# Kernel tuning notes

Hardware: AMD Instinct MI355X
Metric: run time of the kernel (lower is better)

## Reference

```python
import jax, jax.numpy as jnp
import numpy as np

DELTA = 0.0  # default `delta` arg of forward


def _features(voxels, clust_ids, num_clusters):
    # voxels: [N,3] float, clust_ids: [N] int in [0, C)
    n = voxels.shape[0]
    seg = lambda x: jax.ops.segment_sum(x, clust_ids, num_segments=num_clusters)
    counts = seg(jnp.ones((n,), voxels.dtype))                     # [C] cluster sizes
    safe_cnt = jnp.maximum(counts, 1.0)
    center = seg(voxels) / safe_cnt[:, None]                       # [C,3] per-cluster mean
    xc = voxels - center[clust_ids]                                # [N,3] centered voxels
    cov = seg(xc[:, :, None] * xc[:, None, :])                     # [C,3,3] = x^T x per cluster
    w, v = jnp.linalg.eigh(cov)                                    # eigvals ascending (== torch.eig + argsort)
    w2 = w[:, 2]
    dirwt = jnp.where(w2 == 0, 0.0, 1.0 - w[:, 1] / jnp.where(w2 == 0, 1.0, w2))
    wd = w + DELTA
    denom = jnp.where(wd[:, 2] == 0, 1.0, wd[:, 2])
    wn = wd / denom[:, None]                                       # w normalized by largest
    eye = jnp.eye(3, dtype=voxels.dtype)
    B = (1.0 - DELTA) * jnp.einsum('cij,cj,ckj->cik', v, wn, v) + DELTA * eye  # [C,3,3]
    v0 = v[:, :, 2]                                                # [C,3] principal axis
    x0 = jnp.sum(xc * v0[clust_ids], axis=-1)                      # [N] projection on v0
    xp0 = xc - x0[:, None] * v0[clust_ids]                         # [N,3] residual
    np0 = jnp.linalg.norm(xp0, axis=1)                             # [N]
    sc = seg(x0 * np0)                                             # [C] sign score
    v0 = jnp.where((sc < 0)[:, None], -v0, v0) * dirwt[:, None]
    # len(c) < 2 branch: center = the voxel itself (mean handles it), B = delta*I, v0 = 0
    small = counts < 2.0
    B = jnp.where(small[:, None, None], DELTA * eye, B)
    v0 = jnp.where(small[:, None], 0.0, v0)
    return jnp.concatenate([center, B.reshape(num_clusters, 9), v0, counts[:, None]], axis=1)  # [C,16]


def setup_inputs() -> dict:
    key = jax.random.key(0)
    k1, k2 = jax.random.split(key)
    n, c = 4000000, 4096
    data = jax.random.normal(k1, (n, 5), dtype=jnp.float32)
    clust_ids = jax.random.randint(k2, (n,), 0, c)
    return {"data": data, "clust_ids": clust_ids, "num_clusters": c}


def reference(data, clust_ids, num_clusters):
    voxels = data[:, :3].astype(jnp.float32)
    return _features(voxels, clust_ids, num_clusters)
```

## Files before the change

### kernel.cpp

```cpp
#include <hip/hip_runtime.h>
#include <math.h>

#define NC 4096
#define OVCAP 131072
#define CAP1 8520

__device__ __forceinline__ int xcd_id() {
    return (int)__builtin_amdgcn_s_getreg(20 | (0 << 6) | ((4 - 1) << 11));
}

__device__ __forceinline__ void solve_cluster(const float mom[10], float* o,
                                              float4* pcv, float4* pvv) {
    float cntf = mom[0];
    double dn  = (double)cntf;
    double inv = 1.0 / fmax(dn, 1.0);
    double cx = mom[1] * inv, cy = mom[2] * inv, cz = mom[3] * inv;

    double a00 = (double)mom[4] - dn * cx * cx;
    double a01 = (double)mom[5] - dn * cx * cy;
    double a02 = (double)mom[6] - dn * cx * cz;
    double a11 = (double)mom[7] - dn * cy * cy;
    double a12 = (double)mom[8] - dn * cy * cz;
    double a22 = (double)mom[9] - dn * cz * cz;

    double q  = (a00 + a11 + a22) / 3.0;
    double p1 = a01 * a01 + a02 * a02 + a12 * a12;
    double b00 = a00 - q, b11 = a11 - q, b22 = a22 - q;
    double p2 = b00 * b00 + b11 * b11 + b22 * b22 + 2.0 * p1;
    double w0, w1, w2;
    if (!(p2 > 0.0)) {
        w0 = w1 = w2 = q;
    } else {
        double p  = sqrt(p2 / 6.0);
        double ip = 1.0 / p;
        double c00 = b00 * ip, c01 = a01 * ip, c02 = a02 * ip;
        double c11 = b11 * ip, c12 = a12 * ip, c22 = b22 * ip;
        double detB = c00 * (c11 * c22 - c12 * c12)
                    - c01 * (c01 * c22 - c12 * c02)
                    + c02 * (c01 * c12 - c11 * c02);
        double r = fmin(1.0, fmax(-1.0, detB * 0.5));
        double phi = acos(r) / 3.0;
        w2 = q + 2.0 * p * cos(phi);
        w0 = q + 2.0 * p * cos(phi + 2.0943951023931953);
        w1 = 3.0 * q - w2 - w0;
    }

    double denom = (w2 == 0.0) ? 1.0 : w2;
    double dirwt = (w2 == 0.0) ? 0.0 : (1.0 - w1 / w2);

    double C00 = a00 - w1, C11 = a11 - w1, C22 = a22 - w1;
    double D00 = a00 - w0, D11 = a11 - w0, D22 = a22 - w0;
    double M00 = C00 * D00 + a01 * a01 + a02 * a02;
    double M10 = a01 * D00 + C11 * a01 + a12 * a02;
    double M20 = a02 * D00 + a12 * a01 + C22 * a02;
    double M01 = C00 * a01 + a01 * D11 + a02 * a12;
    double M11 = a01 * a01 + C11 * D11 + a12 * a12;
    double M21 = a02 * a01 + a12 * D11 + C22 * a12;
    double M02 = C00 * a02 + a01 * a12 + a02 * D22;
    double M12 = a01 * a02 + C11 * a12 + a12 * D22;
    double M22 = a02 * a02 + a12 * a12 + C22 * D22;
    double n0 = M00 * M00 + M10 * M10 + M20 * M20;
    double n1 = M01 * M01 + M11 * M11 + M21 * M21;
    double n2 = M02 * M02 + M12 * M12 + M22 * M22;
    double vx, vy, vz, nn;
    if (n0 >= n1 && n0 >= n2) { vx = M00; vy = M10; vz = M20; nn = n0; }
    else if (n1 >= n2)        { vx = M01; vy = M11; vz = M21; nn = n1; }
    else                      { vx = M02; vy = M12; vz = M22; nn = n2; }
    if (nn > 1e-300) {
        double rn = 1.0 / sqrt(nn);
        vx *= rn; vy *= rn; vz *= rn;
    } else {
        vx = vy = vz = 0.0;
    }

    bool small = cntf < 2.0f;
    float bscale = small ? 0.0f : (float)(1.0 / denom);

    o[0]  = (float)cx;
    o[1]  = (float)cy;
    o[2]  = (float)cz;
    o[3]  = (float)a00 * bscale;
    o[4]  = (float)a01 * bscale;
    o[5]  = (float)a02 * bscale;
    o[6]  = (float)a01 * bscale;
    o[7]  = (float)a11 * bscale;
    o[8]  = (float)a12 * bscale;
    o[9]  = (float)a02 * bscale;
    o[10] = (float)a12 * bscale;
    o[11] = (float)a22 * bscale;
    o[15] = cntf;

    *pcv = make_float4((float)cx, (float)cy, (float)cz, (float)dirwt);
    *pvv = make_float4((float)vx, (float)vy, (float)vz, cntf);
}

__device__ __forceinline__ void ov_spill(float4 d, int id, float4* ov, int* novf,
                                         float* gmom) {
    int ovi = atomicAdd(novf, 1);
    if (ovi < OVCAP) ov[ovi] = d;
    atomicAdd(&gmom[0 * NC + id], 1.0f);
    atomicAdd(&gmom[1 * NC + id], d.x);
    atomicAdd(&gmom[2 * NC + id], d.y);
    atomicAdd(&gmom[3 * NC + id], d.z);
    atomicAdd(&gmom[4 * NC + id], d.x * d.x);
    atomicAdd(&gmom[5 * NC + id], d.x * d.y);
    atomicAdd(&gmom[6 * NC + id], d.x * d.z);
    atomicAdd(&gmom[7 * NC + id], d.y * d.y);
    atomicAdd(&gmom[8 * NC + id], d.y * d.z);
    atomicAdd(&gmom[9 * NC + id], d.z * d.z);
}

__global__ __launch_bounds__(512) void k_p1(const float* __restrict__ data,
                                            const int* __restrict__ ids,
                                            float4* __restrict__ P1,
                                            int* __restrict__ cnt1,
                                            float4* __restrict__ ov,
                                            int* __restrict__ novf,
                                            float* __restrict__ gmom, int n) {
    __shared__ float sbuf[6144];
    __shared__ unsigned short sid[2048];
    __shared__ int h64[64], boff[64], bglob[64];
    float* sx = sbuf;
    float* sy = sbuf + 2048;
    float* sz = sbuf + 4096;
    int tid = threadIdx.x, lane = tid & 63;
    int xcd = xcd_id() & 7;
    int ntiles = (n + 2047) >> 11;
    for (int t = blockIdx.x; t < ntiles; t += gridDim.x) {
        int vbase = t << 11;
        if (tid < 64) h64[tid] = 0;
        __syncthreads();
        float vx[4], vy[4], vz[4];
        int vid[4], vrk[4];
#pragma unroll
        for (int s = 0; s < 4; s++) {
            int v = vbase + (s << 9) + tid;
            if (v < n) {
                vx[s] = data[v * 5 + 0];
                vy[s] = data[v * 5 + 1];
                vz[s] = data[v * 5 + 2];
                int id = ids[v];
                vid[s] = id;
                vrk[s] = atomicAdd(&h64[id >> 6], 1);
            } else vid[s] = -1;
        }
        __syncthreads();
        if (tid < 64) {
            int c0 = h64[tid], sc = c0;
            for (int off = 1; off < 64; off <<= 1) {
                int u = __shfl_up(sc, off);
                if (lane >= off) sc += u;
            }
            boff[tid] = sc - c0;
            bglob[tid] = atomicAdd(&cnt1[((tid << 3) + xcd) << 4], c0);
        }
        __syncthreads();
#pragma unroll
        for (int s = 0; s < 4; s++)
            if (vid[s] >= 0) {
                int p = boff[vid[s] >> 6] + vrk[s];
                sx[p] = vx[s]; sy[p] = vy[s]; sz[p] = vz[s];
                sid[p] = (unsigned short)vid[s];
            }
        __syncthreads();
        int tot = n - vbase;
        tot = tot > 2048 ? 2048 : tot;
        for (int i = tid; i < tot; i += 512) {
            int id = (int)sid[i];
            int b = id >> 6;
            int ofs = bglob[b] + (i - boff[b]);
            float4 d = make_float4(sx[i], sy[i], sz[i], __int_as_float(id));
            if (ofs < CAP1)
                P1[(size_t)((b << 3) + xcd) * CAP1 + ofs] = d;
            else
                ov_spill(d, id, ov, novf, gmom);
        }
        __syncthreads();
    }
}

__global__ __launch_bounds__(512) void k_mom(const float4* __restrict__ P1,
                                             const int* __restrict__ cnt1,
                                             float* __restrict__ gmom) {
    __shared__ float sbuf[6144];
    __shared__ int h64[64], boff[64];
    float* sx = sbuf;
    float* sy = sbuf + 2048;
    float* sz = sbuf + 4096;
    int tid = threadIdx.x, lane = tid & 63, w8 = tid >> 6;
    int xcd = blockIdx.x & 7;
    int rest = blockIdx.x >> 3;
    int bucket = rest & 63;
    int q = rest >> 6;
    int sub = (bucket << 3) + xcd;

    int m1c = cnt1[sub << 4];
    m1c = m1c > CAP1 ? CAP1 : m1c;
    int start = (int)(((long long)m1c * q) >> 1);
    int end   = (int)(((long long)m1c * (q + 1)) >> 1);
    size_t sbase = (size_t)sub * CAP1;

    float creg = 0.0f;
    float m1 = 0, m2 = 0, m3 = 0, m4 = 0, m5 = 0, m6 = 0, m7 = 0, m8 = 0, m9 = 0;

    for (int tb = start; tb < end; tb += 2048) {
        if (tid < 64) h64[tid] = 0;
        __syncthreads();
        float4 vd[4];
        int vcid[4], vrk[4];
#pragma unroll
        for (int s = 0; s < 4; s++) {
            int i = tb + (s << 9) + tid;
            if (i < end) {
                float4 d = P1[sbase + i];
                int cid = __float_as_int(d.w) & 63;
                vd[s] = d; vcid[s] = cid;
                vrk[s] = atomicAdd(&h64[cid], 1);
            } else vcid[s] = -1;
        }
        __syncthreads();
        if (tid < 64) {
            int c0 = h64[tid], sc = c0;
            for (int off = 1; off < 64; off <<= 1) {
                int u = __shfl_up(sc, off);
                if (lane >= off) sc += u;
            }
            boff[tid] = sc - c0;
        }
        __syncthreads();
#pragma unroll
        for (int s = 0; s < 4; s++)
            if (vcid[s] >= 0) {
                int p = boff[vcid[s]] + vrk[s];
                sx[p] = vd[s].x; sy[p] = vd[s].y; sz[p] = vd[s].z;
            }
        __syncthreads();
        int len = h64[lane];
        int bo  = boff[lane];
        if (w8 == 0) creg += (float)len;
        for (int j = w8; j < len; j += 8) {
            float x = sx[bo + j], y = sy[bo + j], z = sz[bo + j];
            m1 += x; m2 += y; m3 += z;
            m4 += x * x; m5 += x * y; m6 += x * z;
            m7 += y * y; m8 += y * z; m9 += z * z;
        }
        __syncthreads();
    }

    float* comb = sbuf;
    float regs[10] = {creg, m1, m2, m3, m4, m5, m6, m7, m8, m9};
#pragma unroll
    for (int k = 0; k < 10; k++)
        comb[(((k << 6) + lane) << 3) + w8] = regs[k];
    __syncthreads();
    for (int i = tid; i < 640; i += 512) {
        int k = i >> 6, c = i & 63;
        float* p = comb + (((k << 6) + c) << 3);
        float v = ((p[0] + p[1]) + (p[2] + p[3])) + ((p[4] + p[5]) + (p[6] + p[7]));
        if (v != 0.0f) atomicAdd(&gmom[k * NC + (bucket << 6) + c], v);
    }
}

__global__ __launch_bounds__(256) void k_scp(const float4* __restrict__ P1,
                                             const int* __restrict__ cnt1,
                                             const float4* __restrict__ pcv,
                                             const float4* __restrict__ ov,
                                             const int* __restrict__ novf,
                                             float* __restrict__ gsc) {
    __shared__ float ssc[2][64];
    int tid = threadIdx.x;
    int half = tid >> 7;
    int xcd = blockIdx.x & 7;
    int rest = blockIdx.x >> 3;
    int bucket = rest & 63;
    int q = rest >> 6;
    int sub = (bucket << 3) + xcd;
    if (tid < 128) ssc[tid >> 6][tid & 63] = 0.0f;
    __syncthreads();
    int m1 = cnt1[sub << 4];
    m1 = m1 > CAP1 ? CAP1 : m1;
    int start = (int)(((long long)m1 * q) >> 2);
    int end   = (int)(((long long)m1 * (q + 1)) >> 2);
    size_t sbase = (size_t)sub * CAP1;
    const float4* tab = pcv + ((size_t)bucket << 7);

    for (int i = start + tid; i < end; i += 256) {
        float4 d = P1[sbase + i];
        int cid = __float_as_int(d.w) & 63;
        float4 c4 = tab[cid * 2];
        float4 v4 = tab[cid * 2 + 1];
        float xc = d.x - c4.x, yc = d.y - c4.y, zc = d.z - c4.z;
        float x0 = xc * v4.x + yc * v4.y + zc * v4.z;
        float px = xc - x0 * v4.x;
        float py = yc - x0 * v4.y;
        float pz = zc - x0 * v4.z;
        atomicAdd(&ssc[half][cid], x0 * sqrtf(px * px + py * py + pz * pz));
    }
    if (xcd == 0 && q == 0) {
        int mo = *novf;
        mo = mo > OVCAP ? OVCAP : mo;
        for (int i = tid; i < mo; i += 256) {
            float4 d = ov[i];
            int id = __float_as_int(d.w);
            if ((id >> 6) == bucket) {
                int cid = id & 63;
                float4 c4 = tab[cid * 2];
                float4 v4 = tab[cid * 2 + 1];
                float xc = d.x - c4.x, yc = d.y - c4.y, zc = d.z - c4.z;
                float x0 = xc * v4.x + yc * v4.y + zc * v4.z;
                float px = xc - x0 * v4.x;
                float py = yc - x0 * v4.y;
                float pz = zc - x0 * v4.z;
                atomicAdd(&ssc[half][cid], x0 * sqrtf(px * px + py * py + pz * pz));
            }
        }
    }
    __syncthreads();
    if (tid < 64) {
        float v = ssc[0][tid] + ssc[1][tid];
        if (v != 0.0f) atomicAdd(&gsc[(bucket << 6) + tid], v);
    }
}

__global__ void k_eigen_fb(const float* __restrict__ gmom, float* __restrict__ out,
                           float4* __restrict__ pcv) {
    int c = blockIdx.x * blockDim.x + threadIdx.x;
    if (c >= NC) return;
    float mom[10];
#pragma unroll
    for (int k = 0; k < 10; k++) mom[k] = gmom[k * NC + c];
    solve_cluster(mom, out + c * 16, &pcv[2 * c], &pcv[2 * c + 1]);
}

__global__ void k_final_fb(const float4* __restrict__ pcv,
                           const float* __restrict__ gsc, float* __restrict__ out) {
    int c = blockIdx.x * blockDim.x + threadIdx.x;
    if (c >= NC) return;
    float4 c4 = pcv[2 * c];
    float4 v4 = pcv[2 * c + 1];
    float s = (gsc[c] < 0.0f) ? -c4.w : c4.w;
    if (v4.w < 2.0f) s = 0.0f;
    out[c * 16 + 12] = v4.x * s;
    out[c * 16 + 13] = v4.y * s;
    out[c * 16 + 14] = v4.z * s;
}

__global__ __launch_bounds__(1024) void k_accum_raw(const float* __restrict__ data,
                                                    const int* __restrict__ ids,
                                                    float* __restrict__ gmom, int n) {
    extern __shared__ float s[];
    for (int i = threadIdx.x; i < 10 * NC; i += blockDim.x) s[i] = 0.0f;
    __syncthreads();
    int stride = gridDim.x * blockDim.x;
    for (int i = blockIdx.x * blockDim.x + threadIdx.x; i < n; i += stride) {
        int id = ids[i];
        float x = data[i * 5 + 0], y = data[i * 5 + 1], z = data[i * 5 + 2];
        atomicAdd(&s[0 * NC + id], 1.0f);
        atomicAdd(&s[1 * NC + id], x);
        atomicAdd(&s[2 * NC + id], y);
        atomicAdd(&s[3 * NC + id], z);
        atomicAdd(&s[4 * NC + id], x * x);
        atomicAdd(&s[5 * NC + id], x * y);
        atomicAdd(&s[6 * NC + id], x * z);
        atomicAdd(&s[7 * NC + id], y * y);
        atomicAdd(&s[8 * NC + id], y * z);
        atomicAdd(&s[9 * NC + id], z * z);
    }
    __syncthreads();
    for (int i = threadIdx.x; i < 10 * NC; i += blockDim.x) {
        float v = s[i];
        if (v != 0.0f) atomicAdd(&gmom[i], v);
    }
}

__global__ __launch_bounds__(1024) void k_sc_raw(const float* __restrict__ data,
                                                 const int* __restrict__ ids,
                                                 const float4* __restrict__ pcv,
                                                 float* __restrict__ gsc, int n) {
    extern __shared__ float4 sl4[];
    float4* spc = sl4;
    float4* spv = sl4 + NC;
    float*  ssc = (float*)(sl4 + 2 * NC);
    for (int i = threadIdx.x; i < NC; i += blockDim.x) {
        spc[i] = pcv[2 * i]; spv[i] = pcv[2 * i + 1]; ssc[i] = 0.0f;
    }
    __syncthreads();
    int stride = gridDim.x * blockDim.x;
    for (int i = blockIdx.x * blockDim.x + threadIdx.x; i < n; i += stride) {
        int id = ids[i];
        float4 c4 = spc[id];
        float4 v4 = spv[id];
        float xc = data[i * 5 + 0] - c4.x;
        float yc = data[i * 5 + 1] - c4.y;
        float zc = data[i * 5 + 2] - c4.z;
        float x0 = xc * v4.x + yc * v4.y + zc * v4.z;
        float px = xc - x0 * v4.x;
        float py = yc - x0 * v4.y;
        float pz = zc - x0 * v4.z;
        atomicAdd(&ssc[id], x0 * sqrtf(px * px + py * py + pz * pz));
    }
    __syncthreads();
    for (int i = threadIdx.x; i < NC; i += blockDim.x) {
        float v = ssc[i];
        if (v != 0.0f) atomicAdd(&gsc[i], v);
    }
}

extern "C" void kernel_launch(void* const* d_in, const int* in_sizes, int n_in,
                              void* d_out, int out_size, void* d_ws, size_t ws_size,
                              hipStream_t stream) {
    const float* data = (const float*)d_in[0];
    const int*   ids  = (const int*)d_in[1];
    float* out = (float*)d_out;
    int n = in_sizes[1];

    char* ws = (char*)d_ws;
    float*  gmom = (float*)(ws);
    float*  gsc  = (float*)(ws + 163840);
    int*    cnt1 = (int*)(ws + 180224);
    int*    novf = (int*)(ws + 212992);
    float4* pcv  = (float4*)(ws + 213056);
    float4* ov   = (float4*)(ws + 344128);
    const size_t FIXED = 2441280;
    const size_t P1SZ  = (size_t)512 * CAP1 * 16;

    if (ws_size >= FIXED + P1SZ) {
        float4* P1 = (float4*)(ws + FIXED);
        hipMemsetAsync(ws, 0, 213056, stream);
        hipLaunchKernelGGL(k_p1, dim3(1024), dim3(512), 0, stream,
                           data, ids, P1, cnt1, ov, novf, gmom, n);
        hipLaunchKernelGGL(k_mom, dim3(1024), dim3(512), 0, stream,
                           P1, cnt1, gmom);
        hipLaunchKernelGGL(k_eigen_fb, dim3(16), dim3(256), 0, stream,
                           gmom, out, pcv);
        hipLaunchKernelGGL(k_scp, dim3(2048), dim3(256), 0, stream,
                           P1, cnt1, pcv, ov, novf, gsc);
        hipLaunchKernelGGL(k_final_fb, dim3(16), dim3(256), 0, stream,
                           pcv, gsc, out);
    } else {
        hipMemsetAsync(ws, 0, 180224, stream);
        hipLaunchKernelGGL(k_accum_raw, dim3(256), dim3(1024), 10 * NC * 4, stream,
                           data, ids, gmom, n);
        hipLaunchKernelGGL(k_eigen_fb, dim3(16), dim3(256), 0, stream, gmom, out, pcv);
        hipLaunchKernelGGL(k_sc_raw, dim3(256), dim3(1024), 2 * NC * 16 + NC * 4, stream,
                           data, ids, pcv, gsc, n);
        hipLaunchKernelGGL(k_final_fb, dim3(16), dim3(256), 0, stream, pcv, gsc, out);
    }
}
```

Before: 188.6 us.

## Store bucketed points as SoA with 16-bit ids and double grid splits

The intermediate bucketed point buffer changes from float4 records (x,y,z,id) to separate x, y, z float arrays plus a 16-bit id array. This cuts the bytes written by the partition kernel and read by the moment and sign-score kernels from 16 to 14 per point. The moment and score kernels also split each sub-bucket into twice as many chunks with doubled grids, for more parallelism. The cost is four narrower scattered stores instead of one vector store, and more blocks doing atomic merges.

```diff
diff --git a/kernel.cpp b/kernel.cpp
--- a/kernel.cpp
+++ b/kernel.cpp
@@ -112,7 +112,10 @@
 
 __global__ __launch_bounds__(512) void k_p1(const float* __restrict__ data,
                                             const int* __restrict__ ids,
-                                            float4* __restrict__ P1,
+                                            float* __restrict__ P1x,
+                                            float* __restrict__ P1y,
+                                            float* __restrict__ P1z,
+                                            unsigned short* __restrict__ P1id,
                                             int* __restrict__ cnt1,
                                             float4* __restrict__ ov,
                                             int* __restrict__ novf,
@@ -169,17 +172,23 @@
             int id = (int)sid[i];
             int b = id >> 6;
             int ofs = bglob[b] + (i - boff[b]);
-            float4 d = make_float4(sx[i], sy[i], sz[i], __int_as_float(id));
-            if (ofs < CAP1)
-                P1[(size_t)((b << 3) + xcd) * CAP1 + ofs] = d;
-            else
-                ov_spill(d, id, ov, novf, gmom);
-        }
-        __syncthreads();
-    }
-}
-
-__global__ __launch_bounds__(512) void k_mom(const float4* __restrict__ P1,
+            if (ofs < CAP1) {
+                size_t o = (size_t)((b << 3) + xcd) * CAP1 + ofs;
+                P1x[o] = sx[i]; P1y[o] = sy[i]; P1z[o] = sz[i];
+                P1id[o] = (unsigned short)id;
+            } else {
+                ov_spill(make_float4(sx[i], sy[i], sz[i], __int_as_float(id)),
+                         id, ov, novf, gmom);
+            }
+        }
+        __syncthreads();
+    }
+}
+
+__global__ __launch_bounds__(512) void k_mom(const float* __restrict__ P1x,
+                                             const float* __restrict__ P1y,
+                                             const float* __restrict__ P1z,
+                                             const unsigned short* __restrict__ P1id,
                                              const int* __restrict__ cnt1,
                                              float* __restrict__ gmom) {
     __shared__ float sbuf[6144];
@@ -196,8 +205,8 @@
 
     int m1c = cnt1[sub << 4];
     m1c = m1c > CAP1 ? CAP1 : m1c;
-    int start = (int)(((long long)m1c * q) >> 1);
-    int end   = (int)(((long long)m1c * (q + 1)) >> 1);
+    int start = (int)(((long long)m1c * q) >> 2);
+    int end   = (int)(((long long)m1c * (q + 1)) >> 2);
     size_t sbase = (size_t)sub * CAP1;
 
     float creg = 0.0f;
@@ -206,15 +215,17 @@
     for (int tb = start; tb < end; tb += 2048) {
         if (tid < 64) h64[tid] = 0;
         __syncthreads();
-        float4 vd[4];
+        float vX[4], vY[4], vZ[4];
         int vcid[4], vrk[4];
 #pragma unroll
         for (int s = 0; s < 4; s++) {
             int i = tb + (s << 9) + tid;
             if (i < end) {
-                float4 d = P1[sbase + i];
-                int cid = __float_as_int(d.w) & 63;
-                vd[s] = d; vcid[s] = cid;
+                vX[s] = P1x[sbase + i];
+                vY[s] = P1y[sbase + i];
+                vZ[s] = P1z[sbase + i];
+                int cid = (int)P1id[sbase + i] & 63;
+                vcid[s] = cid;
                 vrk[s] = atomicAdd(&h64[cid], 1);
             } else vcid[s] = -1;
         }
@@ -232,7 +243,7 @@
         for (int s = 0; s < 4; s++)
             if (vcid[s] >= 0) {
                 int p = boff[vcid[s]] + vrk[s];
-                sx[p] = vd[s].x; sy[p] = vd[s].y; sz[p] = vd[s].z;
+                sx[p] = vX[s]; sy[p] = vY[s]; sz[p] = vZ[s];
             }
         __syncthreads();
         int len = h64[lane];
@@ -261,7 +272,10 @@
     }
 }
 
-__global__ __launch_bounds__(256) void k_scp(const float4* __restrict__ P1,
+__global__ __launch_bounds__(256) void k_scp(const float* __restrict__ P1x,
+                                             const float* __restrict__ P1y,
+                                             const float* __restrict__ P1z,
+                                             const unsigned short* __restrict__ P1id,
                                              const int* __restrict__ cnt1,
                                              const float4* __restrict__ pcv,
                                              const float4* __restrict__ ov,
@@ -279,17 +293,17 @@
     __syncthreads();
     int m1 = cnt1[sub << 4];
     m1 = m1 > CAP1 ? CAP1 : m1;
-    int start = (int)(((long long)m1 * q) >> 2);
-    int end   = (int)(((long long)m1 * (q + 1)) >> 2);
+    int start = (int)(((long long)m1 * q) >> 3);
+    int end   = (int)(((long long)m1 * (q + 1)) >> 3);
     size_t sbase = (size_t)sub * CAP1;
     const float4* tab = pcv + ((size_t)bucket << 7);
 
     for (int i = start + tid; i < end; i += 256) {
-        float4 d = P1[sbase + i];
-        int cid = __float_as_int(d.w) & 63;
+        float x = P1x[sbase + i], y = P1y[sbase + i], z = P1z[sbase + i];
+        int cid = (int)P1id[sbase + i] & 63;
         float4 c4 = tab[cid * 2];
         float4 v4 = tab[cid * 2 + 1];
-        float xc = d.x - c4.x, yc = d.y - c4.y, zc = d.z - c4.z;
+        float xc = x - c4.x, yc = y - c4.y, zc = z - c4.z;
         float x0 = xc * v4.x + yc * v4.y + zc * v4.z;
         float px = xc - x0 * v4.x;
         float py = yc - x0 * v4.y;
@@ -422,19 +436,23 @@
     float4* pcv  = (float4*)(ws + 213056);
     float4* ov   = (float4*)(ws + 344128);
     const size_t FIXED = 2441280;
-    const size_t P1SZ  = (size_t)512 * CAP1 * 16;
+    const size_t P1ARR = (size_t)512 * CAP1 * 4;
+    const size_t P1SZ  = 3 * P1ARR + (size_t)512 * CAP1 * 2;
 
     if (ws_size >= FIXED + P1SZ) {
-        float4* P1 = (float4*)(ws + FIXED);
+        float* P1x = (float*)(ws + FIXED);
+        float* P1y = (float*)(ws + FIXED + P1ARR);
+        float* P1z = (float*)(ws + FIXED + 2 * P1ARR);
+        unsigned short* P1id = (unsigned short*)(ws + FIXED + 3 * P1ARR);
         hipMemsetAsync(ws, 0, 213056, stream);
         hipLaunchKernelGGL(k_p1, dim3(1024), dim3(512), 0, stream,
-                           data, ids, P1, cnt1, ov, novf, gmom, n);
-        hipLaunchKernelGGL(k_mom, dim3(1024), dim3(512), 0, stream,
-                           P1, cnt1, gmom);
+                           data, ids, P1x, P1y, P1z, P1id, cnt1, ov, novf, gmom, n);
+        hipLaunchKernelGGL(k_mom, dim3(2048), dim3(512), 0, stream,
+                           P1x, P1y, P1z, P1id, cnt1, gmom);
         hipLaunchKernelGGL(k_eigen_fb, dim3(16), dim3(256), 0, stream,
                            gmom, out, pcv);
-        hipLaunchKernelGGL(k_scp, dim3(2048), dim3(256), 0, stream,
-                           P1, cnt1, pcv, ov, novf, gsc);
+        hipLaunchKernelGGL(k_scp, dim3(4096), dim3(256), 0, stream,
+                           P1x, P1y, P1z, P1id, cnt1, pcv, ov, novf, gsc);
         hipLaunchKernelGGL(k_final_fb, dim3(16), dim3(256), 0, stream,
                            pcv, gsc, out);
     } else {
```

New measurement: 195.8 us. 1.04x slower.
